# Kernel optimization log

Measured on AMD Instinct MI355X. Metric: run time of the kernel, lower is better.

Reference implementation:

```python
import jax, jax.numpy as jnp
import numpy as np
from jax import lax

B_, N_, DIM, HID, DST, NT, IR, DTR, HH, WW = 16, 4096, 192, 384, 16, 17, 128, 24, 64, 64


def _selective_scan(u, delta, A, Bs, Cs, D, delta_bias):
    # u, delta: (B, Din, L); A: (Din, N); Bs, Cs: (B, N, L); D, delta_bias: (Din,)
    delta = jax.nn.softplus(delta + delta_bias[None, :, None])
    dT = jnp.moveaxis(delta, 2, 0)   # (L, B, Din)
    uT = jnp.moveaxis(u, 2, 0)       # (L, B, Din)
    BT = jnp.moveaxis(Bs, 2, 0)      # (L, B, N)
    CT = jnp.moveaxis(Cs, 2, 0)      # (L, B, N)
    Bsz, Din, L = u.shape
    Nst = A.shape[1]
    h0 = jnp.zeros((Bsz, Din, Nst), u.dtype)

    def step(h, inp):
        d_l, u_l, b_l, c_l = inp
        da = jnp.exp(d_l[:, :, None] * A[None])              # (B, Din, N)
        h = da * h + (d_l * u_l)[:, :, None] * b_l[:, None, :]
        y = jnp.einsum('bdn,bn->bd', h, c_l)
        return h, y

    _, ys = lax.scan(step, h0, (dT, uT, BT, CT))
    y = jnp.moveaxis(ys, 0, 2)                               # (B, Din, L)
    return y + u * D[None, :, None]


def _assm_forward(x, token_weight, gumbel_noise, embB, route_w1, route_b1, route_w2,
                  route_b2, inproj_w, inproj_b, cpe_w, cpe_b, x_proj_w, dt_w, dt_b,
                  A_logs, Ds, norm_g, norm_b, outproj_w, outproj_b, H, W, gather_type):
    B, n, C = x.shape
    hidden = inproj_w.shape[0]
    dst = token_weight.shape[1]
    dtr = dt_w.shape[1]

    # routing + gumbel-softmax (hard, straight-through)
    full_emb = embB @ token_weight                           # (NT, d_state)
    hmid = jax.nn.gelu(x @ route_w1.T + route_b1)
    logits = jax.nn.log_softmax(hmid @ route_w2.T + route_b2, axis=-1)
    y_soft = jax.nn.softmax(logits + gumbel_noise, axis=-1)
    idx = jnp.argmax(y_soft, axis=-1)                        # (B, n)
    y_hard = jax.nn.one_hot(idx, logits.shape[-1], dtype=y_soft.dtype)
    cls_policy = y_hard + y_soft - lax.stop_gradient(y_soft)
    prompt = cls_policy @ full_emb                           # (B, n, d_state)

    det = lax.stop_gradient(idx)
    # (gather_type 3/5 keypoint-group remap omitted: gather_type == 1 here)
    sort_idx = jnp.argsort(det, axis=-1)                     # (B, n)
    inv_idx = jnp.argsort(sort_idx, axis=-1)                 # index_reverse

    # in_proj (1x1 conv == pointwise linear) then depthwise CPE gate
    xi = x @ inproj_w.T + inproj_b                           # (B, n, hidden)
    xg = xi.reshape(B, H, W, hidden).transpose(0, 3, 1, 2)   # NCHW
    cpe = lax.conv_general_dilated(xg, cpe_w, (1, 1), 'SAME',
                                   feature_group_count=hidden,
                                   dimension_numbers=('NCHW', 'OIHW', 'NCHW'))
    cpe = cpe + cpe_b[None, :, None, None]
    xg = xg * jax.nn.sigmoid(cpe)
    xflat = xg.reshape(B, hidden, n).transpose(0, 2, 1)      # (B, n, hidden)

    sem_x = jnp.take_along_axis(xflat, sort_idx[:, :, None], axis=1)

    # Selective_Scan core
    xs = sem_x.transpose(0, 2, 1)                            # (B, Din, L)
    x_dbl = jnp.einsum('bdl,cd->bcl', xs, x_proj_w)          # (B, dtr+2N, L)
    dts, Bs, Cs = jnp.split(x_dbl, [dtr, dtr + dst], axis=1)
    dts = jnp.einsum('brl,dr->bdl', dts, dt_w)
    if gather_type != 0:
        Cs = Cs + prompt.transpose(0, 2, 1)
    A = -jnp.exp(A_logs)
    y = _selective_scan(xs, dts, A, Bs, Cs, Ds, dt_b)        # (B, Din, L)
    y = y.transpose(0, 2, 1)                                 # (B, L, hidden)

    mu = jnp.mean(y, axis=-1, keepdims=True)
    var = jnp.mean(jnp.square(y - mu), axis=-1, keepdims=True)
    yn = (y - mu) / jnp.sqrt(var + 1e-5) * norm_g + norm_b
    out = yn @ outproj_w.T + outproj_b                       # (B, n, dim)
    out = jnp.take_along_axis(out, inv_idx[:, :, None], axis=1)
    return out


def setup_inputs() -> dict:
    key = jax.random.key(0)
    ks = jax.random.split(key, 16)

    def rn(k, sh, s=0.02):
        return jax.random.normal(k, sh, dtype=jnp.float32) * s

    u = jax.random.uniform(ks[0], (B_, N_, NT), jnp.float32, 1e-6, 1.0 - 1e-6)
    gumbel = -jnp.log(-jnp.log(u))

    # faithful dt bias init (inverse-softplus of log-uniform dt)
    rng = np.random.default_rng(0)
    dt = np.exp(rng.uniform(size=HID) * (np.log(0.1) - np.log(0.001)) + np.log(0.001))
    dt = np.clip(dt, 1e-4, None)
    inv_dt = dt + np.log(-np.expm1(-dt))

    A_logs = jnp.log(jnp.tile(jnp.arange(1, DST + 1, dtype=jnp.float32), (HID, 1)))

    return {
        'x': jax.random.normal(ks[1], (B_, N_, DIM), jnp.float32),
        'token_weight': rn(ks[2], (IR, DST), 0.1),
        'gumbel_noise': gumbel,
        'embB': jax.random.uniform(ks[3], (NT, IR), jnp.float32, -1.0 / NT, 1.0 / NT),
        'route_w1': rn(ks[4], (DIM // 3, DIM)),
        'route_b1': jnp.zeros((DIM // 3,), jnp.float32),
        'route_w2': rn(ks[5], (NT, DIM // 3)),
        'route_b2': jnp.zeros((NT,), jnp.float32),
        'inproj_w': rn(ks[6], (HID, DIM)),
        'inproj_b': jnp.zeros((HID,), jnp.float32),
        'cpe_w': rn(ks[7], (HID, 1, 3, 3), 0.1),
        'cpe_b': jnp.zeros((HID,), jnp.float32),
        'x_proj_w': rn(ks[8], (DTR + 2 * DST, HID)),
        'dt_w': jax.random.uniform(ks[9], (HID, DTR), jnp.float32, -DTR ** -0.5, DTR ** -0.5),
        'dt_b': jnp.asarray(inv_dt, jnp.float32),
        'A_logs': A_logs,
        'Ds': jnp.ones((HID,), jnp.float32),
        'norm_g': jnp.ones((HID,), jnp.float32),
        'norm_b': jnp.zeros((HID,), jnp.float32),
        'outproj_w': rn(ks[10], (DIM, HID)),
        'outproj_b': jnp.zeros((DIM,), jnp.float32),
        'H': HH,
        'W': WW,
        'gather_type': 1,
    }


def reference(x, token_weight, gumbel_noise, embB, route_w1, route_b1, route_w2,
              route_b2, inproj_w, inproj_b, cpe_w, cpe_b, x_proj_w, dt_w, dt_b,
              A_logs, Ds, norm_g, norm_b, outproj_w, outproj_b, H, W, gather_type):
    return _assm_forward(x, token_weight, gumbel_noise, embB, route_w1, route_b1,
                         route_w2, route_b2, inproj_w, inproj_b, cpe_w, cpe_b,
                         x_proj_w, dt_w, dt_b, A_logs, Ds, norm_g, norm_b,
                         outproj_w, outproj_b, H, W, gather_type)
```

## Files before the change

kernel.cpp:

```cpp
#include <hip/hip_runtime.h>
#include <math.h>

#define NB 16
#define NL 4096
#define ND 192
#define NH 384
#define NS 16
#define NTK 17
#define NIR 128
#define NR 24
#define NHH 64
#define NWW 64
#define NCHUNKS 32
#define CHUNKLEN 128
#define NTOK (NB*NL)

typedef __attribute__((ext_vector_type(8))) short short8;
typedef __attribute__((ext_vector_type(4))) float floatx4;

__device__ __forceinline__ float gelu_tanh(float x){
  return 0.5f*x*(1.0f + tanhf(0.7978845608028654f*(x + 0.044715f*x*x*x)));
}
__device__ __forceinline__ float softplus_f(float x){
  return (x > 20.0f) ? x : log1pf(expf(x));
}
__device__ __forceinline__ short f2bf(float f){
  unsigned u = __float_as_uint(f);
  unsigned r = (u + 0x7fffu + ((u >> 16) & 1u)) >> 16;
  return (short)r;
}

union Pack8 { uint4 v; short s[8]; };

__global__ void k_cvtw(const float* __restrict__ inw, const float* __restrict__ ow,
                       const float* __restrict__ xpw, const float* __restrict__ dtw,
                       short* __restrict__ inwb, short* __restrict__ owb,
                       short* __restrict__ xpwb, short* __restrict__ dtwb,
                       const float* __restrict__ embB, const float* __restrict__ tw,
                       float* __restrict__ fe){
  int i = blockIdx.x*256 + threadIdx.x;
  int stride = gridDim.x*256;
  for (int p = i; p < NH*ND; p += stride) inwb[p] = f2bf(inw[p]);
  for (int p = i; p < ND*NH; p += stride) owb[p] = f2bf(ow[p]);
  for (int p = i; p < 56*NH; p += stride) xpwb[p] = f2bf(xpw[p]);
  for (int p = i; p < NH*32; p += stride){
    int r = p >> 5, c = p & 31;
    dtwb[p] = (c < NR) ? f2bf(dtw[r*NR + c]) : (short)0;
  }
  if (blockIdx.x == 0){
    for (int o = threadIdx.x; o < NTK*NS; o += 256){
      int t = o / NS, s = o % NS;
      float acc = 0.f;
      for (int k = 0; k < NIR; ++k) acc += embB[t*NIR+k]*tw[k*NS+s];
      fe[o] = acc;
    }
  }
}

__global__ __launch_bounds__(256) void k_route(const float* __restrict__ A,
    const float* __restrict__ W, const float* __restrict__ b1,
    const float* __restrict__ w2, const float* __restrict__ b2,
    const float* __restrict__ gumbel, int* __restrict__ idx){
  __shared__ float As[16][68];
  __shared__ float Ws[16][68];
  __shared__ float hm[64*65];
  __shared__ float w2s[NTK*64];
  int tid = threadIdx.x;
  int m0 = blockIdx.x*64;
  int tx = tid & 15, ty = tid >> 4;
  int srow = tid >> 2, skseg = (tid & 3)*4;
  for (int p = tid; p < NTK*64; p += 256) w2s[p] = w2[p];
  float acc[4][4] = {};
  for (int k0 = 0; k0 < ND; k0 += 16){
    {
      const float* ap = A + (size_t)(m0+srow)*ND + k0 + skseg;
      float4 v = *(const float4*)ap;
      As[skseg+0][srow]=v.x; As[skseg+1][srow]=v.y;
      As[skseg+2][srow]=v.z; As[skseg+3][srow]=v.w;
    }
    {
      float4 v = *(const float4*)(W + (size_t)srow*ND + k0 + skseg);
      Ws[skseg+0][srow]=v.x; Ws[skseg+1][srow]=v.y;
      Ws[skseg+2][srow]=v.z; Ws[skseg+3][srow]=v.w;
    }
    __syncthreads();
    #pragma unroll
    for (int kk = 0; kk < 16; ++kk){
      float4 av = *(const float4*)&As[kk][ty*4];
      float4 wv = *(const float4*)&Ws[kk][tx*4];
      acc[0][0] += av.x*wv.x; acc[0][1] += av.x*wv.y;
      acc[0][2] += av.x*wv.z; acc[0][3] += av.x*wv.w;
      acc[1][0] += av.y*wv.x; acc[1][1] += av.y*wv.y;
      acc[1][2] += av.y*wv.z; acc[1][3] += av.y*wv.w;
      acc[2][0] += av.z*wv.x; acc[2][1] += av.z*wv.y;
      acc[2][2] += av.z*wv.z; acc[2][3] += av.z*wv.w;
      acc[3][0] += av.w*wv.x; acc[3][1] += av.w*wv.y;
      acc[3][2] += av.w*wv.z; acc[3][3] += av.w*wv.w;
    }
    __syncthreads();
  }
  #pragma unroll
  for (int i = 0; i < 4; ++i)
    #pragma unroll
    for (int j = 0; j < 4; ++j)
      hm[(ty*4+i)*65 + tx*4+j] = gelu_tanh(acc[i][j] + b1[tx*4+j]);
  __syncthreads();
  if (tid < 64){
    int g = m0 + tid;
    const float* hr = &hm[tid*65];
    float best = -INFINITY; int bi = 0;
    for (int c = 0; c < NTK; ++c){
      float s = b2[c] + gumbel[(size_t)g*NTK + c];
      #pragma unroll
      for (int j = 0; j < 64; ++j) s += hr[j]*w2s[c*64+j];
      if (s > best){ best = s; bi = c; }
    }
    idx[g] = bi;
  }
}

template<int EPI, int AF32, int LNA>
__global__ __launch_bounds__(256) void k_mfma(const void* __restrict__ Aptr, int lda,
    const short* __restrict__ Wbf, int ldw, const float* __restrict__ bias,
    float* __restrict__ C, int ldc, int N, int K, const int* __restrict__ remap,
    const float* __restrict__ lnm, const float* __restrict__ lnr,
    const float* __restrict__ lng, const float* __restrict__ lnb){
  __shared__ short As[128*40];
  __shared__ short Bs[64*40];
  int tid = threadIdx.x;
  int m0 = blockIdx.x*128, n0 = blockIdx.y*64;
  int w = tid >> 6, lane = tid & 63;
  int lq = lane >> 4, lr = lane & 15;
  floatx4 acc[2][4];
  #pragma unroll
  for (int i = 0; i < 2; ++i)
    #pragma unroll
    for (int j = 0; j < 4; ++j) acc[i][j] = (floatx4){0.f,0.f,0.f,0.f};
  int ar = tid >> 1, aq = (tid & 1)*2;
  int br = tid >> 2, bq = tid & 3;
  float mr = 0.f, rr = 0.f;
  if (LNA){ mr = lnm[m0+ar]; rr = lnr[m0+ar]; }
  for (int k0 = 0; k0 < K; k0 += 32){
    Pack8 sa0, sa1;
    if (AF32){
      const float* ap = (const float*)Aptr + (size_t)(m0+ar)*lda + k0 + aq*8;
      float f[16];
      float4 f0 = *(const float4*)(ap);
      float4 f1 = *(const float4*)(ap+4);
      float4 f2 = *(const float4*)(ap+8);
      float4 f3 = *(const float4*)(ap+12);
      f[0]=f0.x; f[1]=f0.y; f[2]=f0.z; f[3]=f0.w;
      f[4]=f1.x; f[5]=f1.y; f[6]=f1.z; f[7]=f1.w;
      f[8]=f2.x; f[9]=f2.y; f[10]=f2.z; f[11]=f2.w;
      f[12]=f3.x; f[13]=f3.y; f[14]=f3.z; f[15]=f3.w;
      if (LNA){
        const float* gp = lng + k0 + aq*8;
        const float* bp = lnb + k0 + aq*8;
        #pragma unroll
        for (int j = 0; j < 16; ++j) f[j] = (f[j]-mr)*rr*gp[j] + bp[j];
      }
      #pragma unroll
      for (int j = 0; j < 8; ++j){ sa0.s[j] = f2bf(f[j]); sa1.s[j] = f2bf(f[8+j]); }
    } else {
      const short* ap = (const short*)Aptr + (size_t)(m0+ar)*lda + k0 + aq*8;
      sa0.v = *(const uint4*)ap;
      sa1.v = *(const uint4*)(ap + 8);
    }
    uint4 bv = {0u,0u,0u,0u};
    if (n0 + br < N) bv = *(const uint4*)(Wbf + (size_t)(n0+br)*ldw + k0 + bq*8);
    __syncthreads();
    *(uint4*)&As[ar*40 + aq*8]     = sa0.v;
    *(uint4*)&As[ar*40 + aq*8 + 8] = sa1.v;
    *(uint4*)&Bs[br*40 + bq*8]     = bv;
    __syncthreads();
    short8 a0 = *(const short8*)&As[(w*32      + lr)*40 + lq*8];
    short8 a1 = *(const short8*)&As[(w*32 + 16 + lr)*40 + lq*8];
    short8 b0 = *(const short8*)&Bs[(     lr)*40 + lq*8];
    short8 b1 = *(const short8*)&Bs[(16 + lr)*40 + lq*8];
    short8 b2 = *(const short8*)&Bs[(32 + lr)*40 + lq*8];
    short8 b3 = *(const short8*)&Bs[(48 + lr)*40 + lq*8];
    acc[0][0] = __builtin_amdgcn_mfma_f32_16x16x32_bf16(a0, b0, acc[0][0], 0,0,0);
    acc[0][1] = __builtin_amdgcn_mfma_f32_16x16x32_bf16(a0, b1, acc[0][1], 0,0,0);
    acc[0][2] = __builtin_amdgcn_mfma_f32_16x16x32_bf16(a0, b2, acc[0][2], 0,0,0);
    acc[0][3] = __builtin_amdgcn_mfma_f32_16x16x32_bf16(a0, b3, acc[0][3], 0,0,0);
    acc[1][0] = __builtin_amdgcn_mfma_f32_16x16x32_bf16(a1, b0, acc[1][0], 0,0,0);
    acc[1][1] = __builtin_amdgcn_mfma_f32_16x16x32_bf16(a1, b1, acc[1][1], 0,0,0);
    acc[1][2] = __builtin_amdgcn_mfma_f32_16x16x32_bf16(a1, b2, acc[1][2], 0,0,0);
    acc[1][3] = __builtin_amdgcn_mfma_f32_16x16x32_bf16(a1, b3, acc[1][3], 0,0,0);
  }
  #pragma unroll
  for (int mt = 0; mt < 2; ++mt){
    #pragma unroll
    for (int r = 0; r < 4; ++r){
      int m = m0 + w*32 + mt*16 + lq*4 + r;
      int orow = (EPI==3) ? remap[m] : m;
      #pragma unroll
      for (int nt = 0; nt < 4; ++nt){
        int n = n0 + nt*16 + lr;
        if (n < N){
          float v = acc[mt][nt][r] + (bias ? bias[n] : 0.f);
          if (EPI==2) v = softplus_f(v);
          C[(size_t)orow*ldc + n] = v;
        }
      }
    }
  }
}

__global__ __launch_bounds__(256) void k_xdbl(const float* __restrict__ us,
    const short* __restrict__ xpwb, const int* __restrict__ idx,
    const float* __restrict__ fe, const int* __restrict__ gt,
    float* __restrict__ Bsb, float* __restrict__ Csb, short* __restrict__ dtsb){
  __shared__ short As[128*40];
  __shared__ short Bs[64*40];
  int tid = threadIdx.x;
  int m0 = blockIdx.x*128;
  int w = tid >> 6, lane = tid & 63;
  int lq = lane >> 4, lr = lane & 15;
  floatx4 acc[2][4];
  #pragma unroll
  for (int i = 0; i < 2; ++i)
    #pragma unroll
    for (int j = 0; j < 4; ++j) acc[i][j] = (floatx4){0.f,0.f,0.f,0.f};
  int ar = tid >> 1, aq = (tid & 1)*2;
  int br = tid >> 2, bq = tid & 3;
  for (int k0 = 0; k0 < NH; k0 += 32){
    Pack8 sa0, sa1;
    {
      const float* ap = us + (size_t)(m0+ar)*NH + k0 + aq*8;
      float f[16];
      float4 f0 = *(const float4*)(ap);
      float4 f1 = *(const float4*)(ap+4);
      float4 f2 = *(const float4*)(ap+8);
      float4 f3 = *(const float4*)(ap+12);
      f[0]=f0.x; f[1]=f0.y; f[2]=f0.z; f[3]=f0.w;
      f[4]=f1.x; f[5]=f1.y; f[6]=f1.z; f[7]=f1.w;
      f[8]=f2.x; f[9]=f2.y; f[10]=f2.z; f[11]=f2.w;
      f[12]=f3.x; f[13]=f3.y; f[14]=f3.z; f[15]=f3.w;
      #pragma unroll
      for (int j = 0; j < 8; ++j){ sa0.s[j] = f2bf(f[j]); sa1.s[j] = f2bf(f[8+j]); }
    }
    uint4 bv = {0u,0u,0u,0u};
    if (br < 56) bv = *(const uint4*)(xpwb + (size_t)br*NH + k0 + bq*8);
    __syncthreads();
    *(uint4*)&As[ar*40 + aq*8]     = sa0.v;
    *(uint4*)&As[ar*40 + aq*8 + 8] = sa1.v;
    *(uint4*)&Bs[br*40 + bq*8]     = bv;
    __syncthreads();
    short8 a0 = *(const short8*)&As[(w*32      + lr)*40 + lq*8];
    short8 a1 = *(const short8*)&As[(w*32 + 16 + lr)*40 + lq*8];
    short8 b0 = *(const short8*)&Bs[(     lr)*40 + lq*8];
    short8 b1 = *(const short8*)&Bs[(16 + lr)*40 + lq*8];
    short8 b2 = *(const short8*)&Bs[(32 + lr)*40 + lq*8];
    short8 b3 = *(const short8*)&Bs[(48 + lr)*40 + lq*8];
    acc[0][0] = __builtin_amdgcn_mfma_f32_16x16x32_bf16(a0, b0, acc[0][0], 0,0,0);
    acc[0][1] = __builtin_amdgcn_mfma_f32_16x16x32_bf16(a0, b1, acc[0][1], 0,0,0);
    acc[0][2] = __builtin_amdgcn_mfma_f32_16x16x32_bf16(a0, b2, acc[0][2], 0,0,0);
    acc[0][3] = __builtin_amdgcn_mfma_f32_16x16x32_bf16(a0, b3, acc[0][3], 0,0,0);
    acc[1][0] = __builtin_amdgcn_mfma_f32_16x16x32_bf16(a1, b0, acc[1][0], 0,0,0);
    acc[1][1] = __builtin_amdgcn_mfma_f32_16x16x32_bf16(a1, b1, acc[1][1], 0,0,0);
    acc[1][2] = __builtin_amdgcn_mfma_f32_16x16x32_bf16(a1, b2, acc[1][2], 0,0,0);
    acc[1][3] = __builtin_amdgcn_mfma_f32_16x16x32_bf16(a1, b3, acc[1][3], 0,0,0);
  }
  int gather = gt[0];
  #pragma unroll
  for (int mt = 0; mt < 2; ++mt){
    #pragma unroll
    for (int r = 0; r < 4; ++r){
      int m = m0 + w*32 + mt*16 + lq*4 + r;
      int id = idx[m];
      #pragma unroll
      for (int nt = 0; nt < 4; ++nt){
        int n = nt*16 + lr;
        float v = acc[mt][nt][r];
        if (n < 24){
          dtsb[(size_t)m*32 + n] = f2bf(v);
        } else if (n < 40){
          Bsb[(size_t)m*NS + (n-24)] = v;
          if (n < 32) dtsb[(size_t)m*32 + n] = 0;
        } else if (n < 56){
          float cv = v;
          if (gather != 0) cv += fe[id*NS + (n-40)];
          Csb[(size_t)m*NS + (n-40)] = cv;
        }
      }
    }
  }
}

__global__ __launch_bounds__(256) void k_sort(const int* __restrict__ idx,
    int* __restrict__ rmap, int* __restrict__ inv){
  int b = blockIdx.x, t = threadIdx.x;
  __shared__ int hist[NTK][256];
  __shared__ int tot[NTK];
  __shared__ int keybase[NTK];
  int keys[16];
  const int* ip = idx + b*NL + t*16;
  #pragma unroll
  for (int i = 0; i < 16; ++i) keys[i] = ip[i];
  #pragma unroll
  for (int k = 0; k < NTK; ++k){
    int c = 0;
    #pragma unroll
    for (int i = 0; i < 16; ++i) c += (keys[i]==k) ? 1 : 0;
    hist[k][t] = c;
  }
  __syncthreads();
  if (t < NTK){
    int run = 0;
    for (int j = 0; j < 256; ++j){ int v = hist[t][j]; hist[t][j] = run; run += v; }
    tot[t] = run;
  }
  __syncthreads();
  if (t == 0){
    int base = 0;
    for (int k = 0; k < NTK; ++k){ keybase[k] = base; base += tot[k]; }
  }
  __syncthreads();
  #pragma unroll
  for (int i = 0; i < 16; ++i){
    int k = keys[i];
    int cb = 0;
    #pragma unroll
    for (int j = 0; j < 16; ++j) cb += (j < i && keys[j]==k) ? 1 : 0;
    int pos = keybase[k] + hist[k][t] + cb;
    rmap[b*NL + pos] = b*NL + t*16 + i;
    inv[b*NL + t*16 + i] = pos;
  }
}

__global__ __launch_bounds__(384) void k_cpe(const float* __restrict__ xi,
    const float* __restrict__ cw, const float* __restrict__ cb,
    const int* __restrict__ inv, float* __restrict__ us){
  int bl = blockIdx.x;
  int cg = bl & 3;
  int xt = (bl>>2) & 7;
  int yt = (bl>>5) & 7;
  int b  = bl >> 8;
  __shared__ float tile[10*10*96];
  int tx = threadIdx.x;
  int ty = threadIdx.y;
  int c0 = cg*96;
  int ch = c0 + tx;
  for (int yy = 0; yy < 10; ++yy){
    int gy = yt*8 + yy - 1;
    for (int xx = ty; xx < 10; xx += 4){
      int gx = xt*8 + xx - 1;
      float v = 0.f;
      if (gy >= 0 && gy < NHH && gx >= 0 && gx < NWW)
        v = xi[((size_t)(b*NL + gy*NWW + gx))*NH + ch];
      tile[(yy*10 + xx)*96 + tx] = v;
    }
  }
  float wreg[9];
  #pragma unroll
  for (int j = 0; j < 9; ++j) wreg[j] = cw[ch*9 + j];
  float bias = cb[ch];
  __syncthreads();
  for (int yy = ty; yy < 8; yy += 4){
    #pragma unroll
    for (int xx = 0; xx < 8; ++xx){
      float acc = bias;
      #pragma unroll
      for (int dy = 0; dy < 3; ++dy)
        #pragma unroll
        for (int dx = 0; dx < 3; ++dx)
          acc += tile[((yy+dy)*10 + (xx+dx))*96 + tx] * wreg[dy*3+dx];
      float center = tile[((yy+1)*10 + (xx+1))*96 + tx];
      float gate = 1.f/(1.f + expf(-acc));
      int l = (yt*8+yy)*NWW + xt*8+xx;
      int pos = inv[b*NL + l];
      us[((size_t)(b*NL + pos))*NH + ch] = center*gate;
    }
  }
}

__device__ __forceinline__ void decay16(bool pw, float dlt, const float* An, float* a){
  if (pw){
    float r  = __expf(dlt*An[0]);
    float r2 = r*r;
    float r3 = r2*r;
    float r4 = r2*r2;
    float r8 = r4*r4;
    float r12 = r8*r4;
    a[0]=r;     a[1]=r2;     a[2]=r3;     a[3]=r4;
    a[4]=r4*r;  a[5]=r4*r2;  a[6]=r4*r3;  a[7]=r8;
    a[8]=r8*r;  a[9]=r8*r2;  a[10]=r8*r3; a[11]=r12;
    a[12]=r12*r; a[13]=r12*r2; a[14]=r12*r3; a[15]=r8*r8;
  } else {
    #pragma unroll
    for (int n = 0; n < NS; ++n) a[n] = __expf(dlt*An[n]);
  }
}
__device__ __forceinline__ bool pwcheck(const float* An){
  bool pw = true;
  #pragma unroll
  for (int n = 1; n < NS; ++n)
    pw = pw && (fabsf(An[n] - (n+1)*An[0]) <= 1e-4f*fabsf(An[n]));
  return pw;
}

__global__ __launch_bounds__(384) void k_scan1(const float* __restrict__ delta,
    const float* __restrict__ us, const float* __restrict__ Bsb,
    const float* __restrict__ A_logs, float* __restrict__ sds, float* __restrict__ Boff){
  int bc = blockIdx.x;
  int c = bc & (NCHUNKS-1);
  int b = bc >> 5;
  int d = threadIdx.x;
  __shared__ float4 Bsh[CHUNKLEN*4];
  int base = b*NL + c*CHUNKLEN;
  {
    const float4* Bg = (const float4*)(Bsb + (size_t)base*NS);
    for (int p = d; p < CHUNKLEN*4; p += 384) Bsh[p] = Bg[p];
  }
  float An[NS];
  #pragma unroll
  for (int n = 0; n < NS; ++n) An[n] = -expf(A_logs[d*NS + n]);
  bool pw = pwcheck(An);
  float h[NS];
  #pragma unroll
  for (int n = 0; n < NS; ++n) h[n]=0.f;
  float sd = 0.f;
  __syncthreads();
  size_t gi = (size_t)base*NH + d;
  float dlt = delta[gi];
  float uv  = us[gi];
  #pragma unroll 2
  for (int s = 0; s < CHUNKLEN; ++s){
    float dltc = dlt, uvc = uv;
    if (s < CHUNKLEN-1){
      dlt = delta[gi + NH];
      uv  = us[gi + NH];
    }
    float du = dltc*uvc;
    sd += dltc;
    float a[NS];
    decay16(pw, dltc, An, a);
    float bb[NS];
    #pragma unroll
    for (int q = 0; q < 4; ++q) *(float4*)&bb[4*q] = Bsh[s*4 + q];
    #pragma unroll
    for (int n = 0; n < NS; ++n) h[n] = a[n]*h[n] + du*bb[n];
    gi += NH;
  }
  sds[(size_t)bc*NH + d] = sd;
  size_t o = ((size_t)bc*NH + d)*NS;
  *(float4*)(Boff + o)      = make_float4(h[0], h[1], h[2], h[3]);
  *(float4*)(Boff + o + 4)  = make_float4(h[4], h[5], h[6], h[7]);
  *(float4*)(Boff + o + 8)  = make_float4(h[8], h[9], h[10],h[11]);
  *(float4*)(Boff + o + 12) = make_float4(h[12],h[13],h[14],h[15]);
}

__global__ __launch_bounds__(256) void k_scan2(const float* __restrict__ A_logs,
    const float* __restrict__ sds, float* __restrict__ Boff){
  int i = blockIdx.x*256 + threadIdx.x;
  int dn = i % (NH*NS);
  int b = i / (NH*NS);
  float An = -expf(A_logs[dn]);
  int d = dn >> 4;
  float h = 0.f;
  for (int c = 0; c < NCHUNKS; ++c){
    int bc = b*NCHUNKS + c;
    float sd = sds[(size_t)bc*NH + d];
    float a = __expf(sd*An);
    size_t o = (size_t)bc*(NH*NS) + dn;
    float bo = Boff[o];
    Boff[o] = h;
    h = a*h + bo;
  }
}

__global__ __launch_bounds__(384) void k_scan3(const float* __restrict__ delta,
    const float* __restrict__ Bsb, const float* __restrict__ Csb,
    const float* __restrict__ A_logs, const float* __restrict__ Ds,
    const float* __restrict__ hinit, float* __restrict__ us,
    float* __restrict__ lnmean, float* __restrict__ lnrstd){
  int bc = blockIdx.x;
  int c = bc & (NCHUNKS-1);
  int b = bc >> 5;
  int d = threadIdx.x;
  __shared__ float4 Bsh[CHUNKLEN*4];
  __shared__ float4 Csh[CHUNKLEN*4];
  __shared__ float ybuf[32*384];
  int base = b*NL + c*CHUNKLEN;
  {
    const float4* Bg = (const float4*)(Bsb + (size_t)base*NS);
    const float4* Cg = (const float4*)(Csb + (size_t)base*NS);
    for (int p = d; p < CHUNKLEN*4; p += 384){
      Bsh[p] = Bg[p];
      Csh[p] = Cg[p];
    }
  }
  float An[NS];
  #pragma unroll
  for (int n = 0; n < NS; ++n) An[n] = -expf(A_logs[d*NS + n]);
  bool pw = pwcheck(An);
  float h[NS];
  size_t ho = ((size_t)bc*NH + d)*NS;
  {
    float4 h0 = *(const float4*)(hinit + ho);
    float4 h1 = *(const float4*)(hinit + ho + 4);
    float4 h2 = *(const float4*)(hinit + ho + 8);
    float4 h3 = *(const float4*)(hinit + ho + 12);
    h[0]=h0.x; h[1]=h0.y; h[2]=h0.z; h[3]=h0.w;
    h[4]=h1.x; h[5]=h1.y; h[6]=h1.z; h[7]=h1.w;
    h[8]=h2.x; h[9]=h2.y; h[10]=h2.z; h[11]=h2.w;
    h[12]=h3.x; h[13]=h3.y; h[14]=h3.z; h[15]=h3.w;
  }
  float Dd = Ds[d];
  int wv = d >> 6, lane = d & 63;
  __syncthreads();
  size_t gi = (size_t)base*NH + d;
  float dlt = delta[gi];
  float uv  = us[gi];
  #pragma unroll 2
  for (int s = 0; s < CHUNKLEN; ++s){
    float dltc = dlt, uvc = uv;
    if (s < CHUNKLEN-1){
      dlt = delta[gi + NH];
      uv  = us[gi + NH];
    }
    float du = dltc*uvc;
    float a[NS];
    decay16(pw, dltc, An, a);
    float bb[NS], cc[NS];
    #pragma unroll
    for (int q = 0; q < 4; ++q){
      *(float4*)&bb[4*q] = Bsh[s*4 + q];
      *(float4*)&cc[4*q] = Csh[s*4 + q];
    }
    #pragma unroll
    for (int n = 0; n < NS; ++n) h[n] = a[n]*h[n] + du*bb[n];
    float ya = 0.f, yb = 0.f, yc = 0.f, yd = 0.f;
    #pragma unroll
    for (int q = 0; q < 4; ++q){
      ya += h[q]*cc[q];
      yb += h[4+q]*cc[4+q];
      yc += h[8+q]*cc[8+q];
      yd += h[12+q]*cc[12+q];
    }
    float y = ((ya+yb)+(yc+yd)) + uvc*Dd;
    us[gi] = y;
    ybuf[(s & 31)*384 + d] = y;
    gi += NH;
    if ((s & 31) == 31){
      __syncthreads();
      int ws0 = s - 31;
      for (int t = wv; t < 32; t += 6){
        const float* rp = &ybuf[t*384];
        float v[6];
        #pragma unroll
        for (int i = 0; i < 6; ++i) v[i] = rp[i*64 + lane];
        float sm = 0.f;
        #pragma unroll
        for (int i = 0; i < 6; ++i) sm += v[i];
        #pragma unroll
        for (int off = 32; off > 0; off >>= 1) sm += __shfl_xor(sm, off);
        float mu = sm * (1.f/NH);
        float vs = 0.f;
        #pragma unroll
        for (int i = 0; i < 6; ++i){ float dv = v[i]-mu; vs += dv*dv; }
        #pragma unroll
        for (int off = 32; off > 0; off >>= 1) vs += __shfl_xor(vs, off);
        float rs = rsqrtf(vs*(1.f/NH) + 1e-5f);
        if (lane == 0){ lnmean[base+ws0+t] = mu; lnrstd[base+ws0+t] = rs; }
      }
      __syncthreads();
    }
  }
}

extern "C" void kernel_launch(void* const* d_in, const int* in_sizes, int n_in,
                              void* d_out, int out_size, void* d_ws, size_t ws_size,
                              hipStream_t stream){
  const float* x      = (const float*)d_in[0];
  const float* tw     = (const float*)d_in[1];
  const float* gumbel = (const float*)d_in[2];
  const float* embB   = (const float*)d_in[3];
  const float* rw1    = (const float*)d_in[4];
  const float* rb1    = (const float*)d_in[5];
  const float* rw2    = (const float*)d_in[6];
  const float* rb2    = (const float*)d_in[7];
  const float* inw    = (const float*)d_in[8];
  const float* inb    = (const float*)d_in[9];
  const float* cw     = (const float*)d_in[10];
  const float* cb     = (const float*)d_in[11];
  const float* xpw    = (const float*)d_in[12];
  const float* dtw    = (const float*)d_in[13];
  const float* dtb    = (const float*)d_in[14];
  const float* A_logs = (const float*)d_in[15];
  const float* Ds     = (const float*)d_in[16];
  const float* ng     = (const float*)d_in[17];
  const float* nbv    = (const float*)d_in[18];
  const float* ow     = (const float*)d_in[19];
  const float* ob     = (const float*)d_in[20];
  const int*   gt     = (const int*)d_in[23];
  float* out = (float*)d_out;

  float* ws = (float*)d_ws;
  size_t o = 0;
  float* fe   = ws + o; o += 512;
  int* idx    = (int*)(ws + o); o += NTOK;
  int* rmap   = (int*)(ws + o); o += NTOK;
  int* inv    = (int*)(ws + o); o += NTOK;
  float* hmid = ws + o; o += (size_t)NTOK*64;
  float* xi   = ws + o; o += (size_t)NTOK*NH;
  float* us   = ws + o; o += (size_t)NTOK*NH;
  float* Bsb  = ws + o; o += (size_t)NTOK*NS;
  float* Csb  = ws + o; o += (size_t)NTOK*NS;
  float* sds  = ws + o; o += (size_t)NB*NCHUNKS*NH;
  float* Bof  = ws + o; o += (size_t)NB*NCHUNKS*NH*NS;
  short* inwb = (short*)(ws + o); o += (NH*ND)/2;
  short* owb  = (short*)(ws + o); o += (ND*NH)/2;
  short* xpwb = (short*)(ws + o); o += (56*NH)/2 + 32;
  short* dtwb = (short*)(ws + o); o += (NH*32)/2;
  float* delta = xi;
  short* dtsb = (short*)Bof;
  float* lnmean = (float*)idx;
  float* lnrstd = (float*)inv;
  (void)hmid;

  k_cvtw<<<64,256,0,stream>>>(inw, ow, xpw, dtw, inwb, owb, xpwb, dtwb, embB, tw, fe);
  k_route<<<NTOK/64,256,0,stream>>>(x, rw1, rb1, rw2, rb2, gumbel, idx);
  k_sort<<<NB,256,0,stream>>>(idx, rmap, inv);
  k_mfma<0,1,0><<<dim3(NTOK/128,6),256,0,stream>>>(x, ND, inwb, ND, inb, xi, NH, NH, ND,
      nullptr, nullptr, nullptr, nullptr, nullptr);
  k_cpe<<<NB*64*4,dim3(96,4),0,stream>>>(xi, cw, cb, inv, us);
  k_xdbl<<<NTOK/128,256,0,stream>>>(us, xpwb, idx, fe, gt, Bsb, Csb, dtsb);
  k_mfma<2,0,0><<<dim3(NTOK/128,6),256,0,stream>>>(dtsb, 32, dtwb, 32, dtb, delta, NH, NH, 32,
      nullptr, nullptr, nullptr, nullptr, nullptr);
  k_scan1<<<NB*NCHUNKS,384,0,stream>>>(delta, us, Bsb, A_logs, sds, Bof);
  k_scan2<<<(NB*NH*NS)/256,256,0,stream>>>(A_logs, sds, Bof);
  k_scan3<<<NB*NCHUNKS,384,0,stream>>>(delta, Bsb, Csb, A_logs, Ds, Bof, us,
                                       lnmean, lnrstd);
  k_mfma<3,1,1><<<dim3(NTOK/128,3),256,0,stream>>>(us, NH, owb, NH, ob, out, ND, ND, NH,
      rmap, lnmean, lnrstd, ng, nbv);
}
```

Measured before the change: 674.4 us.

## Fuse dt projection into x_proj kernel and merge weight-convert with routing

The dt low-rank projection (24->384 plus softplus) now runs inside the x_proj MFMA kernel. The bf16 dt activations stay in shared memory, so the dtsb global round-trip and one kernel launch go away. The weight conversion and routing kernels are merged into a single launch, with block ranges split by role. The cost is fewer blocks in the dt GEMM stage (512 versus 3072) and a serial loop over six N-tiles in each block, which may reduce parallelism.

```diff
diff --git a/kernel.cpp b/kernel.cpp
--- a/kernel.cpp
+++ b/kernel.cpp
@@ -32,54 +32,57 @@
 
 union Pack8 { uint4 v; short s[8]; };
 
-__global__ void k_cvtw(const float* __restrict__ inw, const float* __restrict__ ow,
-                       const float* __restrict__ xpw, const float* __restrict__ dtw,
-                       short* __restrict__ inwb, short* __restrict__ owb,
-                       short* __restrict__ xpwb, short* __restrict__ dtwb,
-                       const float* __restrict__ embB, const float* __restrict__ tw,
-                       float* __restrict__ fe){
-  int i = blockIdx.x*256 + threadIdx.x;
-  int stride = gridDim.x*256;
-  for (int p = i; p < NH*ND; p += stride) inwb[p] = f2bf(inw[p]);
-  for (int p = i; p < ND*NH; p += stride) owb[p] = f2bf(ow[p]);
-  for (int p = i; p < 56*NH; p += stride) xpwb[p] = f2bf(xpw[p]);
-  for (int p = i; p < NH*32; p += stride){
-    int r = p >> 5, c = p & 31;
-    dtwb[p] = (c < NR) ? f2bf(dtw[r*NR + c]) : (short)0;
-  }
-  if (blockIdx.x == 0){
-    for (int o = threadIdx.x; o < NTK*NS; o += 256){
-      int t = o / NS, s = o % NS;
-      float acc = 0.f;
-      for (int k = 0; k < NIR; ++k) acc += embB[t*NIR+k]*tw[k*NS+s];
-      fe[o] = acc;
-    }
-  }
-}
-
-__global__ __launch_bounds__(256) void k_route(const float* __restrict__ A,
-    const float* __restrict__ W, const float* __restrict__ b1,
-    const float* __restrict__ w2, const float* __restrict__ b2,
-    const float* __restrict__ gumbel, int* __restrict__ idx){
+__global__ __launch_bounds__(256) void k_pre(
+    const float* __restrict__ inw, const float* __restrict__ ow,
+    const float* __restrict__ xpw, const float* __restrict__ dtw,
+    short* __restrict__ inwb, short* __restrict__ owb,
+    short* __restrict__ xpwb, short* __restrict__ dtwb,
+    const float* __restrict__ embB, const float* __restrict__ tw,
+    float* __restrict__ fe,
+    const float* __restrict__ x, const float* __restrict__ rw1,
+    const float* __restrict__ rb1, const float* __restrict__ rw2,
+    const float* __restrict__ rb2, const float* __restrict__ gumbel,
+    int* __restrict__ idx){
   __shared__ float As[16][68];
   __shared__ float Ws[16][68];
   __shared__ float hm[64*65];
   __shared__ float w2s[NTK*64];
   int tid = threadIdx.x;
-  int m0 = blockIdx.x*64;
+  int bl = blockIdx.x;
+  if (bl < 64){
+    int i = bl*256 + tid;
+    int stride = 64*256;
+    for (int p = i; p < NH*ND; p += stride) inwb[p] = f2bf(inw[p]);
+    for (int p = i; p < ND*NH; p += stride) owb[p] = f2bf(ow[p]);
+    for (int p = i; p < 56*NH; p += stride) xpwb[p] = f2bf(xpw[p]);
+    for (int p = i; p < NH*32; p += stride){
+      int r = p >> 5, c = p & 31;
+      dtwb[p] = (c < NR) ? f2bf(dtw[r*NR + c]) : (short)0;
+    }
+    if (bl == 0){
+      for (int o = tid; o < NTK*NS; o += 256){
+        int t = o / NS, s = o % NS;
+        float acc = 0.f;
+        for (int k = 0; k < NIR; ++k) acc += embB[t*NIR+k]*tw[k*NS+s];
+        fe[o] = acc;
+      }
+    }
+    return;
+  }
+  int m0 = (bl - 64)*64;
   int tx = tid & 15, ty = tid >> 4;
   int srow = tid >> 2, skseg = (tid & 3)*4;
-  for (int p = tid; p < NTK*64; p += 256) w2s[p] = w2[p];
+  for (int p = tid; p < NTK*64; p += 256) w2s[p] = rw2[p];
   float acc[4][4] = {};
   for (int k0 = 0; k0 < ND; k0 += 16){
     {
-      const float* ap = A + (size_t)(m0+srow)*ND + k0 + skseg;
+      const float* ap = x + (size_t)(m0+srow)*ND + k0 + skseg;
       float4 v = *(const float4*)ap;
       As[skseg+0][srow]=v.x; As[skseg+1][srow]=v.y;
       As[skseg+2][srow]=v.z; As[skseg+3][srow]=v.w;
     }
     {
-      float4 v = *(const float4*)(W + (size_t)srow*ND + k0 + skseg);
+      float4 v = *(const float4*)(rw1 + (size_t)srow*ND + k0 + skseg);
       Ws[skseg+0][srow]=v.x; Ws[skseg+1][srow]=v.y;
       Ws[skseg+2][srow]=v.z; Ws[skseg+3][srow]=v.w;
     }
@@ -103,14 +106,14 @@
   for (int i = 0; i < 4; ++i)
     #pragma unroll
     for (int j = 0; j < 4; ++j)
-      hm[(ty*4+i)*65 + tx*4+j] = gelu_tanh(acc[i][j] + b1[tx*4+j]);
+      hm[(ty*4+i)*65 + tx*4+j] = gelu_tanh(acc[i][j] + rb1[tx*4+j]);
   __syncthreads();
   if (tid < 64){
     int g = m0 + tid;
     const float* hr = &hm[tid*65];
     float best = -INFINITY; int bi = 0;
     for (int c = 0; c < NTK; ++c){
-      float s = b2[c] + gumbel[(size_t)g*NTK + c];
+      float s = rb2[c] + gumbel[(size_t)g*NTK + c];
       #pragma unroll
       for (int j = 0; j < 64; ++j) s += hr[j]*w2s[c*64+j];
       if (s > best){ best = s; bi = c; }
@@ -207,10 +210,11 @@
   }
 }
 
-__global__ __launch_bounds__(256) void k_xdbl(const float* __restrict__ us,
-    const short* __restrict__ xpwb, const int* __restrict__ idx,
+__global__ __launch_bounds__(256) void k_xdd(const float* __restrict__ us,
+    const short* __restrict__ xpwb, const short* __restrict__ dtwb,
+    const float* __restrict__ dtb, const int* __restrict__ idx,
     const float* __restrict__ fe, const int* __restrict__ gt,
-    float* __restrict__ Bsb, float* __restrict__ Csb, short* __restrict__ dtsb){
+    float* __restrict__ Bsb, float* __restrict__ Csb, float* __restrict__ delta){
   __shared__ short As[128*40];
   __shared__ short Bs[64*40];
   int tid = threadIdx.x;
@@ -263,25 +267,64 @@
     acc[1][3] = __builtin_amdgcn_mfma_f32_16x16x32_bf16(a1, b3, acc[1][3], 0,0,0);
   }
   int gather = gt[0];
+  __syncthreads();
   #pragma unroll
   for (int mt = 0; mt < 2; ++mt){
     #pragma unroll
     for (int r = 0; r < 4; ++r){
       int m = m0 + w*32 + mt*16 + lq*4 + r;
+      int ml = m - m0;
       int id = idx[m];
       #pragma unroll
       for (int nt = 0; nt < 4; ++nt){
         int n = nt*16 + lr;
         float v = acc[mt][nt][r];
         if (n < 24){
-          dtsb[(size_t)m*32 + n] = f2bf(v);
+          As[ml*40 + n] = f2bf(v);
         } else if (n < 40){
           Bsb[(size_t)m*NS + (n-24)] = v;
-          if (n < 32) dtsb[(size_t)m*32 + n] = 0;
         } else if (n < 56){
           float cv = v;
           if (gather != 0) cv += fe[id*NS + (n-40)];
           Csb[(size_t)m*NS + (n-40)] = cv;
+        }
+      }
+    }
+  }
+  if (tid < 128) *(uint4*)&As[tid*40 + 24] = (uint4){0u,0u,0u,0u};
+  __syncthreads();
+  short8 a0 = *(const short8*)&As[(w*32      + lr)*40 + lq*8];
+  short8 a1 = *(const short8*)&As[(w*32 + 16 + lr)*40 + lq*8];
+  for (int t6 = 0; t6 < 6; ++t6){
+    if (t6) __syncthreads();
+    *(uint4*)&Bs[br*40 + bq*8] = *(const uint4*)(dtwb + (size_t)(t6*64+br)*32 + bq*8);
+    __syncthreads();
+    short8 b0 = *(const short8*)&Bs[(     lr)*40 + lq*8];
+    short8 b1 = *(const short8*)&Bs[(16 + lr)*40 + lq*8];
+    short8 b2 = *(const short8*)&Bs[(32 + lr)*40 + lq*8];
+    short8 b3 = *(const short8*)&Bs[(48 + lr)*40 + lq*8];
+    floatx4 d0[2][4];
+    #pragma unroll
+    for (int i = 0; i < 2; ++i)
+      #pragma unroll
+      for (int j = 0; j < 4; ++j) d0[i][j] = (floatx4){0.f,0.f,0.f,0.f};
+    d0[0][0] = __builtin_amdgcn_mfma_f32_16x16x32_bf16(a0, b0, d0[0][0], 0,0,0);
+    d0[0][1] = __builtin_amdgcn_mfma_f32_16x16x32_bf16(a0, b1, d0[0][1], 0,0,0);
+    d0[0][2] = __builtin_amdgcn_mfma_f32_16x16x32_bf16(a0, b2, d0[0][2], 0,0,0);
+    d0[0][3] = __builtin_amdgcn_mfma_f32_16x16x32_bf16(a0, b3, d0[0][3], 0,0,0);
+    d0[1][0] = __builtin_amdgcn_mfma_f32_16x16x32_bf16(a1, b0, d0[1][0], 0,0,0);
+    d0[1][1] = __builtin_amdgcn_mfma_f32_16x16x32_bf16(a1, b1, d0[1][1], 0,0,0);
+    d0[1][2] = __builtin_amdgcn_mfma_f32_16x16x32_bf16(a1, b2, d0[1][2], 0,0,0);
+    d0[1][3] = __builtin_amdgcn_mfma_f32_16x16x32_bf16(a1, b3, d0[1][3], 0,0,0);
+    #pragma unroll
+    for (int mt = 0; mt < 2; ++mt){
+      #pragma unroll
+      for (int r = 0; r < 4; ++r){
+        int m = m0 + w*32 + mt*16 + lq*4 + r;
+        #pragma unroll
+        for (int nt = 0; nt < 4; ++nt){
+          int n = t6*64 + nt*16 + lr;
+          delta[(size_t)m*NH + n] = softplus_f(d0[mt][nt][r] + dtb[n]);
         }
       }
     }
@@ -615,20 +658,17 @@
   short* xpwb = (short*)(ws + o); o += (56*NH)/2 + 32;
   short* dtwb = (short*)(ws + o); o += (NH*32)/2;
   float* delta = xi;
-  short* dtsb = (short*)Bof;
   float* lnmean = (float*)idx;
   float* lnrstd = (float*)inv;
   (void)hmid;
 
-  k_cvtw<<<64,256,0,stream>>>(inw, ow, xpw, dtw, inwb, owb, xpwb, dtwb, embB, tw, fe);
-  k_route<<<NTOK/64,256,0,stream>>>(x, rw1, rb1, rw2, rb2, gumbel, idx);
+  k_pre<<<64 + NTOK/64,256,0,stream>>>(inw, ow, xpw, dtw, inwb, owb, xpwb, dtwb,
+      embB, tw, fe, x, rw1, rb1, rw2, rb2, gumbel, idx);
   k_sort<<<NB,256,0,stream>>>(idx, rmap, inv);
   k_mfma<0,1,0><<<dim3(NTOK/128,6),256,0,stream>>>(x, ND, inwb, ND, inb, xi, NH, NH, ND,
       nullptr, nullptr, nullptr, nullptr, nullptr);
   k_cpe<<<NB*64*4,dim3(96,4),0,stream>>>(xi, cw, cb, inv, us);
-  k_xdbl<<<NTOK/128,256,0,stream>>>(us, xpwb, idx, fe, gt, Bsb, Csb, dtsb);
-  k_mfma<2,0,0><<<dim3(NTOK/128,6),256,0,stream>>>(dtsb, 32, dtwb, 32, dtb, delta, NH, NH, 32,
-      nullptr, nullptr, nullptr, nullptr, nullptr);
+  k_xdd<<<NTOK/128,256,0,stream>>>(us, xpwb, dtwb, dtb, idx, fe, gt, Bsb, Csb, delta);
   k_scan1<<<NB*NCHUNKS,384,0,stream>>>(delta, us, Bsb, A_logs, sds, Bof);
   k_scan2<<<(NB*NH*NS)/256,256,0,stream>>>(A_logs, sds, Bof);
   k_scan3<<<NB*NCHUNKS,384,0,stream>>>(delta, Bsb, Csb, A_logs, Ds, Bof, us,
```

New measurement: 695.4 us. +3.1%, slower.
